# Kernel tuning notes

Measured on AMD Instinct MI355X. Metric: run time of the kernel, lower is better.

## Reference

```python
import jax, jax.numpy as jnp
import numpy as np

B, L, D, H = 2, 1024, 1024, 16
DH = D // H
E, ES, K = 32, 128, 4
LN_EPS = 1e-5


def sinusoidal_pos(length, d):
    # relative offsets length-1 .. -(length-1), Transformer-XL convention
    pos = jnp.arange(length - 1, -length, -1, dtype=jnp.float32)  # [2L-1]
    inv = jnp.exp(-jnp.arange(0, d, 2, dtype=jnp.float32) * (np.log(10000.0) / d))
    ang = pos[:, None] * inv[None, :]
    return jnp.concatenate([jnp.sin(ang), jnp.cos(ang)], axis=-1)  # [2L-1, D]


def layer_norm(x, g, b):
    m = jnp.mean(x, -1, keepdims=True)
    v = jnp.mean(jnp.square(x - m), -1, keepdims=True)
    return (x - m) * jax.lax.rsqrt(v + LN_EPS) * g + b


def rel_attention(x, Wq, Wk, Wv, Wo, Wp):
    q = (x @ Wq).reshape(B, L, H, DH).transpose(0, 2, 1, 3)
    k = (x @ Wk).reshape(B, L, H, DH).transpose(0, 2, 1, 3)
    v = (x @ Wv).reshape(B, L, H, DH).transpose(0, 2, 1, 3)
    p = (sinusoidal_pos(L, D) @ Wp).reshape(2 * L - 1, H, DH).transpose(1, 0, 2)  # [H,2L-1,DH]
    ac = jnp.einsum('bhid,bhjd->bhij', q, k)            # content score
    bd = jnp.einsum('bhid,hpd->bhip', q, p)             # position score [B,H,L,2L-1]
    # offset index of key j relative to query i: pos array index = j - i + (L-1)
    idx = jnp.arange(L)[None, :] - jnp.arange(L)[:, None] + (L - 1)  # [L,L]
    bd = jnp.take_along_axis(bd, jnp.broadcast_to(idx[None, None], (B, H, L, L)), axis=-1)
    att = jax.nn.softmax((ac + bd) / np.sqrt(DH), axis=-1)
    out = jnp.einsum('bhij,bhjd->bhid', att, v).transpose(0, 2, 1, 3).reshape(B, L, D)
    return out @ Wo


def moe_ffn(x, sel_w, keys, values):
    t = x.reshape(-1, D)                                # [T, D]
    gates = jax.nn.sigmoid(t @ sel_w)                   # [T, E]
    topv, topi = jax.lax.top_k(gates, K)                # top-k expert selection
    gate = jnp.zeros_like(gates).at[jnp.arange(t.shape[0])[:, None], topi].set(topv)
    h = jax.nn.relu(jnp.einsum('td,edh->teh', t, keys))  # expert up-proj + ReLU
    y = jnp.einsum('teh,te,ehd->td', h, gate, values)    # gated expert down-proj
    return y.reshape(x.shape)


def setup_inputs():
    key = jax.random.key(0)
    ks = jax.random.split(key, 9)
    s = 0.02
    f32 = jnp.float32
    return {
        'src': jax.random.normal(ks[0], (B, L, D), f32),
        'Wq': jax.random.normal(ks[1], (D, D), f32) * s,
        'Wk': jax.random.normal(ks[2], (D, D), f32) * s,
        'Wv': jax.random.normal(ks[3], (D, D), f32) * s,
        'Wo': jax.random.normal(ks[4], (D, D), f32) * s,
        'Wp': jax.random.normal(ks[5], (D, D), f32) * s,
        'ln1_g': jnp.ones((D,), f32),
        'ln1_b': jnp.zeros((D,), f32),
        'ln2_g': jnp.ones((D,), f32),
        'ln2_b': jnp.zeros((D,), f32),
        'sel_w': jax.random.normal(ks[6], (D, E), f32) * s,
        'keys': jax.random.normal(ks[7], (E, D, ES), f32) * s,
        'values': jax.random.normal(ks[8], (E, ES, D), f32) * s,
    }


def reference(src, Wq, Wk, Wv, Wo, Wp, ln1_g, ln1_b, ln2_g, ln2_b, sel_w, keys, values):
    # pre-LN: attn block
    x2 = layer_norm(src, ln1_g, ln1_b)
    x = src + rel_attention(x2, Wq, Wk, Wv, Wo, Wp)
    # pre-LN: MoE FFN block
    x2 = layer_norm(x, ln2_g, ln2_b)
    return x + moe_ffn(x2, sel_w, keys, values)
```

## Files before the change

kernel.cpp:

```cpp
#include <hip/hip_runtime.h>
#include <hip/hip_bf16.h>
#include <cmath>

typedef __attribute__((ext_vector_type(8))) short s16x8;
typedef __attribute__((ext_vector_type(8))) __bf16 bf16x8;
typedef __attribute__((ext_vector_type(4))) float f32x4;

__device__ __forceinline__ float b2f(short u) {
  union { unsigned int u32; float f; } c;
  c.u32 = ((unsigned int)(unsigned short)u) << 16;
  return c.f;
}
__device__ __forceinline__ short f2b(float f) {
  __hip_bfloat16 h = __float2bfloat16(f);
  return *reinterpret_cast<short*>(&h);
}

__device__ __forceinline__ f32x4 mfma16(bf16x8 a, bf16x8 b, f32x4 c) {
  return __builtin_amdgcn_mfma_f32_16x16x32_bf16(a, b, c, 0, 0, 0);
}

__global__ __launch_bounds__(256) void conv_k(const float* __restrict__ in,
                                              short* __restrict__ out, int n) {
  int stride = gridDim.x << 8;
  for (int i = (blockIdx.x << 8) + threadIdx.x; i < n; i += stride)
    out[i] = f2b(in[i]);
}

__global__ __launch_bounds__(256) void pos_k(short* __restrict__ out) {
  int row = blockIdx.x;
  int t = threadIdx.x;
#pragma unroll
  for (int i = 0; i < 4; ++i) {
    int c = t + (i << 8);
    float val = 0.f;
    if (row < 2047) {
      int f = (c < 512) ? c : c - 512;
      float inv = expf(-(float)f * (float)(9.210340371976184 / 512.0));
      float ang = (float)(1023 - row) * inv;
      val = (c < 512) ? sinf(ang) : cosf(ang);
    }
    out[row * 1024 + c] = f2b(val);
  }
}

__global__ __launch_bounds__(256) void ln_k(const float* __restrict__ in,
                                            const float* __restrict__ g,
                                            const float* __restrict__ bb,
                                            short* __restrict__ out) {
  int row = blockIdx.x;
  int t = threadIdx.x;
  float v[4];
#pragma unroll
  for (int i = 0; i < 4; ++i) v[i] = in[row * 1024 + t + (i << 8)];
  __shared__ float red1[4], red2[4];
  float s = v[0] + v[1] + v[2] + v[3];
#pragma unroll
  for (int m = 1; m < 64; m <<= 1) s += __shfl_xor(s, m);
  if ((t & 63) == 0) red1[t >> 6] = s;
  __syncthreads();
  float mean = (red1[0] + red1[1] + red1[2] + red1[3]) * (1.f / 1024.f);
  float d2 = 0.f;
#pragma unroll
  for (int i = 0; i < 4; ++i) { float d = v[i] - mean; d2 += d * d; }
#pragma unroll
  for (int m = 1; m < 64; m <<= 1) d2 += __shfl_xor(d2, m);
  if ((t & 63) == 0) red2[t >> 6] = d2;
  __syncthreads();
  float var = (red2[0] + red2[1] + red2[2] + red2[3]) * (1.f / 1024.f);
  float rstd = rsqrtf(var + 1e-5f);
#pragma unroll
  for (int i = 0; i < 4; ++i) {
    int c = t + (i << 8);
    out[row * 1024 + c] = f2b((v[i] - mean) * rstd * g[c] + bb[c]);
  }
}

#define GD 1024
template <int EP>
__global__ __launch_bounds__(256) void gemm_k(const short* __restrict__ A,
                                              const short* __restrict__ B,
                                              void* __restrict__ outp,
                                              const float* __restrict__ resid) {
  __shared__ __align__(16) short lA[64 * 40];
  __shared__ __align__(16) short lB[64 * 40];
  const int tid = threadIdx.x;
  const int wave = tid >> 6, lane = tid & 63;
  const int wr = wave >> 1, wc = wave & 1;
  const int m0 = blockIdx.y * 64, n0 = blockIdx.x * 64;
  f32x4 acc[2][2] = {};
  const int ar = tid >> 2, ak = (tid & 3) << 3;
  const int bk = tid >> 3, bn = (tid & 7) << 3;
  const int k8 = (lane >> 4) << 3;
  const int rA0 = wr * 32 + (lane & 15);
  const int cB0 = wc * 32 + (lane & 15);
  for (int kt = 0; kt < GD; kt += 32) {
    *(bf16x8*)&lA[ar * 40 + ak] = *(const bf16x8*)&A[(m0 + ar) * GD + kt + ak];
    s16x8 bv = *(const s16x8*)&B[(kt + bk) * GD + n0 + bn];
#pragma unroll
    for (int i = 0; i < 8; ++i) lB[(bn + i) * 40 + bk] = bv[i];
    __syncthreads();
    bf16x8 a0 = *(bf16x8*)&lA[rA0 * 40 + k8];
    bf16x8 a1 = *(bf16x8*)&lA[(rA0 + 16) * 40 + k8];
    bf16x8 b0 = *(bf16x8*)&lB[cB0 * 40 + k8];
    bf16x8 b1 = *(bf16x8*)&lB[(cB0 + 16) * 40 + k8];
    acc[0][0] = mfma16(a0, b0, acc[0][0]);
    acc[0][1] = mfma16(a0, b1, acc[0][1]);
    acc[1][0] = mfma16(a1, b0, acc[1][0]);
    acc[1][1] = mfma16(a1, b1, acc[1][1]);
    __syncthreads();
  }
#pragma unroll
  for (int mi = 0; mi < 2; ++mi)
#pragma unroll
    for (int ni = 0; ni < 2; ++ni)
#pragma unroll
      for (int r = 0; r < 4; ++r) {
        int row = m0 + wr * 32 + mi * 16 + ((lane >> 4) << 2) + r;
        int col = n0 + wc * 32 + ni * 16 + (lane & 15);
        float vv = acc[mi][ni][r];
        if (EP == 0) {
          ((short*)outp)[row * GD + col] = f2b(vv);
        } else if (EP == 1) {
          int b = row >> 10, l = row & 1023, h = col >> 6, dh = col & 63;
          ((short*)outp)[(((b << 4) + h) * 1024 + l) * 64 + dh] = f2b(vv);
        } else {
          ((float*)outp)[row * GD + col] = vv + resid[row * GD + col];
        }
      }
}

#define KP 72
#define VP 72
#define PBP 72
#define TP 84
#define SPP 72
__global__ __launch_bounds__(256) void attn_k(const short* __restrict__ q,
                                              const short* __restrict__ k,
                                              const short* __restrict__ v,
                                              const short* __restrict__ P,
                                              short* __restrict__ out) {
  __shared__ __align__(16) short sK[64 * KP];
  __shared__ __align__(16) short sVT[64 * VP];
  __shared__ __align__(16) short sPB[128 * PBP];
  __shared__ __align__(16) float sT[4 * 16 * TP];
  __shared__ __align__(16) short sP[4 * 16 * SPP];

  const int bx = blockIdx.x;
  const int bh = bx >> 4;
  const int chunk = bx & 15;
  const int b = bh >> 4, h = bh & 15;
  const int i0 = chunk << 6;
  const int t = threadIdx.x;
  const int w = t >> 6;
  const int lane = t & 63;
  const int cl = lane & 15;
  const int g = lane >> 4;
  const size_t base = (size_t)bh << 16;
  const short* qb = q + base;
  const short* kb = k + base;
  const short* vb = v + base;

  bf16x8 qf[2];
  {
    const short* qr = qb + (i0 + w * 16 + cl) * 64 + g * 8;
    qf[0] = *(const bf16x8*)&qr[0];
    qf[1] = *(const bf16x8*)&qr[32];
  }

  f32x4 acc_o[4] = {};
  float m_reg[4], l_reg[4];
#pragma unroll
  for (int r = 0; r < 4; ++r) { m_reg[r] = -1e30f; l_reg[r] = 0.f; }

  float* sTw = sT + w * (16 * TP);
  short* sPw = sP + w * (16 * SPP);
  const int a_row = g * 4;
  const int prow0 = 48 - w * 16 + cl;

  for (int j0 = 0; j0 < 1024; j0 += 64) {
    __syncthreads();
    {
      int c0 = t << 1;
#pragma unroll
      for (int u = 0; u < 2; ++u) {
        int c = c0 + u;
        int row = c >> 3, col8 = (c & 7) << 3;
        *(s16x8*)&sK[row * KP + col8] = *(const s16x8*)&kb[(j0 + row) * 64 + col8];
        s16x8 vv = *(const s16x8*)&vb[(j0 + row) * 64 + col8];
#pragma unroll
        for (int e = 0; e < 8; ++e) sVT[(col8 + e) * VP + row] = vv[e];
      }
      int ob = 960 - i0 + j0;
#pragma unroll
      for (int u = 0; u < 4; ++u) {
        int c = t + (u << 8);
        int row = c >> 3, col8 = (c & 7) << 3;
        *(s16x8*)&sPB[row * PBP + col8] =
            *(const s16x8*)&P[(size_t)(ob + row) * 1024 + (h << 6) + col8];
      }
    }
    __syncthreads();

    f32x4 acc_s[4] = {};
    f32x4 acc_t[5] = {};
#pragma unroll
    for (int kk = 0; kk < 2; ++kk) {
      bf16x8 a = qf[kk];
      int koff = kk * 32 + g * 8;
#pragma unroll
      for (int nj = 0; nj < 4; ++nj) {
        bf16x8 bfr = *(const bf16x8*)&sK[(nj * 16 + cl) * KP + koff];
        acc_s[nj] = mfma16(a, bfr, acc_s[nj]);
      }
#pragma unroll
      for (int nt = 0; nt < 5; ++nt) {
        bf16x8 bfr = *(const bf16x8*)&sPB[(prow0 + nt * 16) * PBP + koff];
        acc_t[nt] = mfma16(a, bfr, acc_t[nt]);
      }
    }
#pragma unroll
    for (int nt = 0; nt < 5; ++nt)
#pragma unroll
      for (int r = 0; r < 4; ++r)
        sTw[(a_row + r) * TP + nt * 16 + cl] = acc_t[nt][r];

    float sval[4][4];
#pragma unroll
    for (int r = 0; r < 4; ++r) {
      int a = a_row + r;
      int abase = a * (TP - 1) + 15 + cl;
      float mr = -1e30f;
#pragma unroll
      for (int ni = 0; ni < 4; ++ni) {
        float sv = (acc_s[ni][r] + sTw[abase + ni * 16]) * 0.125f;
        sval[r][ni] = sv;
        mr = fmaxf(mr, sv);
      }
      mr = fmaxf(mr, __shfl_xor(mr, 1));
      mr = fmaxf(mr, __shfl_xor(mr, 2));
      mr = fmaxf(mr, __shfl_xor(mr, 4));
      mr = fmaxf(mr, __shfl_xor(mr, 8));
      float nm = fmaxf(m_reg[r], mr);
      float sc = __expf(m_reg[r] - nm);
      m_reg[r] = nm;
      float ls = 0.f;
#pragma unroll
      for (int ni = 0; ni < 4; ++ni) {
        float p = __expf(sval[r][ni] - nm);
        sval[r][ni] = p;
        ls += p;
      }
      ls += __shfl_xor(ls, 1);
      ls += __shfl_xor(ls, 2);
      ls += __shfl_xor(ls, 4);
      ls += __shfl_xor(ls, 8);
      l_reg[r] = l_reg[r] * sc + ls;
#pragma unroll
      for (int nd = 0; nd < 4; ++nd) acc_o[nd][r] *= sc;
#pragma unroll
      for (int ni = 0; ni < 4; ++ni)
        sPw[a * SPP + ni * 16 + cl] = f2b(sval[r][ni]);
    }

#pragma unroll
    for (int kk = 0; kk < 2; ++kk) {
      int koff = kk * 32 + g * 8;
      bf16x8 a = *(const bf16x8*)&sPw[cl * SPP + koff];
#pragma unroll
      for (int nd = 0; nd < 4; ++nd) {
        bf16x8 bfr = *(const bf16x8*)&sVT[(nd * 16 + cl) * VP + koff];
        acc_o[nd] = mfma16(a, bfr, acc_o[nd]);
      }
    }
  }
  {
    int orow = b * 1024 + i0 + w * 16 + a_row;
#pragma unroll
    for (int r = 0; r < 4; ++r) {
      float rl = 1.f / l_reg[r];
      int row = orow + r;
#pragma unroll
      for (int nd = 0; nd < 4; ++nd)
        out[row * 1024 + (h << 6) + nd * 16 + cl] = f2b(acc_o[nd][r] * rl);
    }
  }
}

__global__ __launch_bounds__(256) void gate_k(const float* __restrict__ x,
                                              const float* __restrict__ g,
                                              const float* __restrict__ bb,
                                              const float* __restrict__ selw,
                                              float* __restrict__ topv,
                                              int* __restrict__ topi) {
  int tok = blockIdx.x;
  int t = threadIdx.x;
  __shared__ float sT[1024];
  __shared__ float red1[4], red2[4];
  __shared__ float sG[32];
  float v[4];
#pragma unroll
  for (int i = 0; i < 4; ++i) v[i] = x[tok * 1024 + t + (i << 8)];
  float s = v[0] + v[1] + v[2] + v[3];
#pragma unroll
  for (int m = 1; m < 64; m <<= 1) s += __shfl_xor(s, m);
  if ((t & 63) == 0) red1[t >> 6] = s;
  __syncthreads();
  float mean = (red1[0] + red1[1] + red1[2] + red1[3]) * (1.f / 1024.f);
  float d2 = 0.f;
#pragma unroll
  for (int i = 0; i < 4; ++i) { float d = v[i] - mean; d2 += d * d; }
#pragma unroll
  for (int m = 1; m < 64; m <<= 1) d2 += __shfl_xor(d2, m);
  if ((t & 63) == 0) red2[t >> 6] = d2;
  __syncthreads();
  float var = (red2[0] + red2[1] + red2[2] + red2[3]) * (1.f / 1024.f);
  float rstd = rsqrtf(var + 1e-5f);
#pragma unroll
  for (int i = 0; i < 4; ++i) {
    int c = t + (i << 8);
    sT[c] = (v[i] - mean) * rstd * g[c] + bb[c];
  }
  __syncthreads();
  if (t < 32) {
    float acc = 0.f;
    for (int d = 0; d < 1024; ++d) acc += sT[d] * selw[d * 32 + t];
    sG[t] = acc;
  }
  __syncthreads();
  if (t == 0) {
    bool used[32];
    for (int e = 0; e < 32; ++e) used[e] = false;
    for (int kk = 0; kk < 4; ++kk) {
      int bi = 0;
      float bvv = -1e30f;
      for (int e = 0; e < 32; ++e)
        if (!used[e] && sG[e] > bvv) { bvv = sG[e]; bi = e; }
      used[bi] = true;
      topi[tok * 4 + kk] = bi;
      topv[tok * 4 + kk] = 1.f / (1.f + __expf(-bvv));
    }
  }
}

__global__ __launch_bounds__(256) void moe_k(const short* __restrict__ x2,
                                             const float* __restrict__ xres,
                                             const short* __restrict__ keys,
                                             const short* __restrict__ vals,
                                             const float* __restrict__ topv,
                                             const int* __restrict__ topi,
                                             float* __restrict__ out) {
  int tok = blockIdx.x;
  int t = threadIdx.x;
  __shared__ float sT[1024];
  __shared__ float sHp[2][128];
  __shared__ float sH[128];
#pragma unroll
  for (int i = 0; i < 4; ++i) sT[t + (i << 8)] = b2f(x2[tok * 1024 + t + (i << 8)]);
  float y[4] = {0.f, 0.f, 0.f, 0.f};
  __syncthreads();
  for (int kk = 0; kk < 4; ++kk) {
    int e = topi[tok * 4 + kk];
    float g = topv[tok * 4 + kk];
    int s = t & 127, half = t >> 7;
    const short* kp = keys + (size_t)e * 1024 * 128 + s;
    float acc = 0.f;
    int d0 = half << 9;
    for (int d = d0; d < d0 + 512; ++d) acc += sT[d] * b2f(kp[(size_t)d * 128]);
    sHp[half][s] = acc;
    __syncthreads();
    if (t < 128) sH[t] = fmaxf(sHp[0][t] + sHp[1][t], 0.f);
    __syncthreads();
    const short* vp = vals + (size_t)e * 128 * 1024;
#pragma unroll
    for (int u = 0; u < 4; ++u) {
      int d = t + (u << 8);
      float acc2 = 0.f;
      for (int s2 = 0; s2 < 128; ++s2) acc2 += sH[s2] * b2f(vp[s2 * 1024 + d]);
      y[u] += g * acc2;
    }
    __syncthreads();
  }
#pragma unroll
  for (int u = 0; u < 4; ++u) {
    int d = t + (u << 8);
    out[tok * 1024 + d] = xres[tok * 1024 + d] + y[u];
  }
}

extern "C" void kernel_launch(void* const* d_in, const int* in_sizes, int n_in,
                              void* d_out, int out_size, void* d_ws, size_t ws_size,
                              hipStream_t stream) {
  const float* src = (const float*)d_in[0];
  const float* ln1g = (const float*)d_in[6];
  const float* ln1b = (const float*)d_in[7];
  const float* ln2g = (const float*)d_in[8];
  const float* ln2b = (const float*)d_in[9];
  const float* selw = (const float*)d_in[10];

  char* ws = (char*)d_ws;
  short* x2a = (short*)(ws + (size_t)0);
  short* pos = (short*)(ws + ((size_t)4 << 20));
  short* P = (short*)(ws + ((size_t)8 << 20));
  short* q = (short*)(ws + ((size_t)12 << 20));
  short* k = (short*)(ws + ((size_t)16 << 20));
  short* v = (short*)(ws + ((size_t)20 << 20));
  short* ao = (short*)(ws + ((size_t)24 << 20));
  short* x2b = (short*)(ws + ((size_t)28 << 20));
  float* x = (float*)(ws + ((size_t)32 << 20));
  float* topv = (float*)(ws + ((size_t)40 << 20));
  int* topi = (int*)(ws + ((size_t)40 << 20) + (32 << 10));
  short* cWq = (short*)(ws + ((size_t)41 << 20));
  short* cWk = (short*)(ws + ((size_t)43 << 20));
  short* cWv = (short*)(ws + ((size_t)45 << 20));
  short* cWo = (short*)(ws + ((size_t)47 << 20));
  short* cWp = (short*)(ws + ((size_t)49 << 20));
  short* cKeys = (short*)(ws + ((size_t)51 << 20));
  short* cVals = (short*)(ws + ((size_t)59 << 20));

  conv_k<<<512, 256, 0, stream>>>((const float*)d_in[1], cWq, 1048576);
  conv_k<<<512, 256, 0, stream>>>((const float*)d_in[2], cWk, 1048576);
  conv_k<<<512, 256, 0, stream>>>((const float*)d_in[3], cWv, 1048576);
  conv_k<<<512, 256, 0, stream>>>((const float*)d_in[4], cWo, 1048576);
  conv_k<<<512, 256, 0, stream>>>((const float*)d_in[5], cWp, 1048576);
  conv_k<<<1024, 256, 0, stream>>>((const float*)d_in[11], cKeys, 4194304);
  conv_k<<<1024, 256, 0, stream>>>((const float*)d_in[12], cVals, 4194304);

  dim3 gg(16, 32);
  pos_k<<<2048, 256, 0, stream>>>(pos);
  ln_k<<<2048, 256, 0, stream>>>(src, ln1g, ln1b, x2a);
  gemm_k<1><<<gg, 256, 0, stream>>>(x2a, cWq, q, nullptr);
  gemm_k<1><<<gg, 256, 0, stream>>>(x2a, cWk, k, nullptr);
  gemm_k<1><<<gg, 256, 0, stream>>>(x2a, cWv, v, nullptr);
  gemm_k<0><<<gg, 256, 0, stream>>>(pos, cWp, P, nullptr);
  attn_k<<<512, 256, 0, stream>>>(q, k, v, P, ao);
  gemm_k<2><<<gg, 256, 0, stream>>>(ao, cWo, x, src);
  ln_k<<<2048, 256, 0, stream>>>(x, ln2g, ln2b, x2b);
  gate_k<<<2048, 256, 0, stream>>>(x, ln2g, ln2b, selw, topv, topi);
  moe_k<<<2048, 256, 0, stream>>>(x2b, x, cKeys, cVals, topv, topi, (float*)d_out);
}
```

Before: 685.8 us.

## Bucket tokens per expert and run MoE as grouped MFMA GEMMs

Replaces the per-token scalar MoE kernel with an expert-bucketing pass (atomic counters building per-expert token and gate lists), followed by grouped up-projection and down-projection kernels that use bf16 MFMA tiles over 64 tokens per block. The down-projection scatters gated results into the output with float atomicAdd after the residual is copied in. This removes the redundant per-token reloads of expert weights and the scalar FMA loops. In exchange it adds atomics, which make the summation order nondeterministic, plus a few extra launches and padded tiles for experts with few tokens.

```diff
diff --git a/kernel.cpp b/kernel.cpp
--- a/kernel.cpp
+++ b/kernel.cpp
@@ -343,48 +343,156 @@
   }
 }
 
-__global__ __launch_bounds__(256) void moe_k(const short* __restrict__ x2,
-                                             const float* __restrict__ xres,
-                                             const short* __restrict__ keys,
-                                             const short* __restrict__ vals,
-                                             const float* __restrict__ topv,
-                                             const int* __restrict__ topi,
-                                             float* __restrict__ out) {
-  int tok = blockIdx.x;
-  int t = threadIdx.x;
-  __shared__ float sT[1024];
-  __shared__ float sHp[2][128];
-  __shared__ float sH[128];
-#pragma unroll
-  for (int i = 0; i < 4; ++i) sT[t + (i << 8)] = b2f(x2[tok * 1024 + t + (i << 8)]);
-  float y[4] = {0.f, 0.f, 0.f, 0.f};
-  __syncthreads();
+#define CAP 2048
+__global__ __launch_bounds__(32) void zero_k(int* __restrict__ cnt) {
+  cnt[threadIdx.x] = 0;
+}
+__global__ __launch_bounds__(256) void bucket_k(const int* __restrict__ topi,
+                                                const float* __restrict__ topv,
+                                                int* __restrict__ cnt,
+                                                int* __restrict__ toklist,
+                                                float* __restrict__ gatelist) {
+  int tok = (blockIdx.x << 8) + threadIdx.x;
+#pragma unroll
   for (int kk = 0; kk < 4; ++kk) {
     int e = topi[tok * 4 + kk];
-    float g = topv[tok * 4 + kk];
-    int s = t & 127, half = t >> 7;
-    const short* kp = keys + (size_t)e * 1024 * 128 + s;
-    float acc = 0.f;
-    int d0 = half << 9;
-    for (int d = d0; d < d0 + 512; ++d) acc += sT[d] * b2f(kp[(size_t)d * 128]);
-    sHp[half][s] = acc;
-    __syncthreads();
-    if (t < 128) sH[t] = fmaxf(sHp[0][t] + sHp[1][t], 0.f);
-    __syncthreads();
-    const short* vp = vals + (size_t)e * 128 * 1024;
+    float gv = topv[tok * 4 + kk];
+    int pos = atomicAdd(&cnt[e], 1);
+    toklist[e * CAP + pos] = tok;
+    gatelist[e * CAP + pos] = gv;
+  }
+}
+
+__global__ __launch_bounds__(256) void cp_k(const float* __restrict__ in,
+                                            float* __restrict__ out) {
+  int i = (blockIdx.x << 8) + threadIdx.x;
+  *(f32x4*)&out[i << 2] = *(const f32x4*)&in[i << 2];
+}
+
+__global__ __launch_bounds__(256) void moe_up_k(const short* __restrict__ x2,
+                                                const short* __restrict__ keys,
+                                                const int* __restrict__ cnt,
+                                                const int* __restrict__ toklist,
+                                                short* __restrict__ hbuf) {
+  const int e = blockIdx.y;
+  const int n = cnt[e];
+  const int t0 = blockIdx.x << 6;
+  if (t0 >= n) return;
+  __shared__ int stok[64];
+  __shared__ __align__(16) short lA[64 * 36];
+  __shared__ __align__(16) short lB[128 * 36];
+  const int tid = threadIdx.x;
+  if (tid < 64) {
+    int idx = t0 + tid;
+    stok[tid] = toklist[e * CAP + (idx < n ? idx : n - 1)];
+  }
+  __syncthreads();
+  const int w = tid >> 6, lane = tid & 63, cl = lane & 15, g = lane >> 4;
+  const int ar = tid >> 2, ak = (tid & 3) << 3;
+  const int bkr = tid >> 3, bc0 = (tid & 7) << 4;
+  const short* kbase = keys + ((size_t)e << 17);
+  f32x4 acc[8] = {};
+  for (int kt = 0; kt < 1024; kt += 32) {
+    if (kt) __syncthreads();
+    *(s16x8*)&lA[ar * 36 + ak] = *(const s16x8*)&x2[stok[ar] * 1024 + kt + ak];
+    {
+      s16x8 b0 = *(const s16x8*)&kbase[(kt + bkr) * 128 + bc0];
+      s16x8 b1 = *(const s16x8*)&kbase[(kt + bkr) * 128 + bc0 + 8];
+#pragma unroll
+      for (int i2 = 0; i2 < 8; ++i2) {
+        lB[(bc0 + i2) * 36 + bkr] = b0[i2];
+        lB[(bc0 + 8 + i2) * 36 + bkr] = b1[i2];
+      }
+    }
+    __syncthreads();
+    bf16x8 a = *(const bf16x8*)&lA[(w * 16 + cl) * 36 + g * 8];
+#pragma unroll
+    for (int nt = 0; nt < 8; ++nt) {
+      bf16x8 bfr = *(const bf16x8*)&lB[(nt * 16 + cl) * 36 + g * 8];
+      acc[nt] = mfma16(a, bfr, acc[nt]);
+    }
+  }
+#pragma unroll
+  for (int nt = 0; nt < 8; ++nt)
+#pragma unroll
+    for (int r = 0; r < 4; ++r) {
+      int lrow = w * 16 + g * 4 + r;
+      if (t0 + lrow < n)
+        hbuf[(size_t)(e * CAP + t0 + lrow) * 128 + nt * 16 + cl] =
+            f2b(fmaxf(acc[nt][r], 0.f));
+    }
+}
+
+__global__ __launch_bounds__(256) void moe_down_k(const short* __restrict__ hbuf,
+                                                  const short* __restrict__ vals,
+                                                  const int* __restrict__ cnt,
+                                                  const int* __restrict__ toklist,
+                                                  const float* __restrict__ gatelist,
+                                                  float* __restrict__ out) {
+  const int e = blockIdx.y;
+  const int n = cnt[e];
+  const int t0 = blockIdx.x << 6;
+  if (t0 >= n) return;
+  __shared__ int stok[64];
+  __shared__ float sgate[64];
+  __shared__ __align__(16) short lA[64 * 132];
+  __shared__ __align__(16) short lB[64 * 132];
+  const int tid = threadIdx.x;
+  if (tid < 64) {
+    int idx = t0 + tid;
+    int ci = idx < n ? idx : n - 1;
+    stok[tid] = toklist[e * CAP + ci];
+    sgate[tid] = gatelist[e * CAP + ci];
+  }
+  {
+    int ar = tid >> 2, ac0 = (tid & 3) << 3;
+    const short* hr = &hbuf[(size_t)(e * CAP + t0 + ar) * 128];
+#pragma unroll
+    for (int u = 0; u < 4; ++u)
+      *(s16x8*)&lA[ar * 132 + ac0 + u * 32] = *(const s16x8*)&hr[ac0 + u * 32];
+  }
+  const int w = tid >> 6, lane = tid & 63, cl = lane & 15, g = lane >> 4;
+  const short* vbase = vals + ((size_t)e << 17);
+  const int bkr = tid >> 1, bc0 = (tid & 1) << 5;
+  __syncthreads();
+  bf16x8 afr[4];
+#pragma unroll
+  for (int ks = 0; ks < 4; ++ks)
+    afr[ks] = *(const bf16x8*)&lA[(w * 16 + cl) * 132 + ks * 32 + g * 8];
+  float gates[4];
+  int stokr[4];
+  bool valid[4];
+#pragma unroll
+  for (int r = 0; r < 4; ++r) {
+    int lrow = w * 16 + g * 4 + r;
+    gates[r] = sgate[lrow];
+    stokr[r] = stok[lrow];
+    valid[r] = (t0 + lrow) < n;
+  }
+  for (int nc = 0; nc < 16; ++nc) {
+    __syncthreads();
 #pragma unroll
     for (int u = 0; u < 4; ++u) {
-      int d = t + (u << 8);
-      float acc2 = 0.f;
-      for (int s2 = 0; s2 < 128; ++s2) acc2 += sH[s2] * b2f(vp[s2 * 1024 + d]);
-      y[u] += g * acc2;
-    }
-    __syncthreads();
-  }
-#pragma unroll
-  for (int u = 0; u < 4; ++u) {
-    int d = t + (u << 8);
-    out[tok * 1024 + d] = xres[tok * 1024 + d] + y[u];
+      s16x8 bv = *(const s16x8*)&vbase[bkr * 1024 + nc * 64 + bc0 + u * 8];
+#pragma unroll
+      for (int i2 = 0; i2 < 8; ++i2) lB[(bc0 + u * 8 + i2) * 132 + bkr] = bv[i2];
+    }
+    __syncthreads();
+    f32x4 acc[4] = {};
+#pragma unroll
+    for (int ks = 0; ks < 4; ++ks)
+#pragma unroll
+      for (int nt = 0; nt < 4; ++nt) {
+        bf16x8 bfr = *(const bf16x8*)&lB[(nt * 16 + cl) * 132 + ks * 32 + g * 8];
+        acc[nt] = mfma16(afr[ks], bfr, acc[nt]);
+      }
+#pragma unroll
+    for (int nt = 0; nt < 4; ++nt)
+#pragma unroll
+      for (int r = 0; r < 4; ++r)
+        if (valid[r])
+          atomicAdd(&out[stokr[r] * 1024 + nc * 64 + nt * 16 + cl],
+                    gates[r] * acc[nt][r]);
   }
 }
 
@@ -417,6 +525,10 @@
   short* cWp = (short*)(ws + ((size_t)49 << 20));
   short* cKeys = (short*)(ws + ((size_t)51 << 20));
   short* cVals = (short*)(ws + ((size_t)59 << 20));
+  short* hbuf = q;
+  int* cnt = (int*)(ws + ((size_t)4 << 20));
+  int* toklist = (int*)(ws + ((size_t)4 << 20) + (4 << 10));
+  float* gatelist = (float*)(ws + ((size_t)4 << 20) + (512 << 10));
 
   conv_k<<<512, 256, 0, stream>>>((const float*)d_in[1], cWq, 1048576);
   conv_k<<<512, 256, 0, stream>>>((const float*)d_in[2], cWk, 1048576);
@@ -437,5 +549,10 @@
   gemm_k<2><<<gg, 256, 0, stream>>>(ao, cWo, x, src);
   ln_k<<<2048, 256, 0, stream>>>(x, ln2g, ln2b, x2b);
   gate_k<<<2048, 256, 0, stream>>>(x, ln2g, ln2b, selw, topv, topi);
-  moe_k<<<2048, 256, 0, stream>>>(x2b, x, cKeys, cVals, topv, topi, (float*)d_out);
-}
+  zero_k<<<1, 32, 0, stream>>>(cnt);
+  bucket_k<<<8, 256, 0, stream>>>(topi, topv, cnt, toklist, gatelist);
+  cp_k<<<2048, 256, 0, stream>>>(x, (float*)d_out);
+  moe_up_k<<<dim3(32, 32), 256, 0, stream>>>(x2b, cKeys, cnt, toklist, hbuf);
+  moe_down_k<<<dim3(32, 32), 256, 0, stream>>>(hbuf, cVals, cnt, toklist, gatelist,
+                                               (float*)d_out);
+}
```

Result: faster. 566.7 us (-17.4%).
